# Kernel tuning notes

Measured on AMD Instinct MI355X. Metric: run time of the kernel, lower is better.

The kernel has to match this reference:

```python
import jax, jax.numpy as jnp
import numpy as np

CLAMP_MIN = 1e-6
CLAMP_MAX = 1e6


def setup_inputs() -> dict:
    key = jax.random.key(0)
    k1, k2, k3, k4, k5 = jax.random.split(key, 5)
    R, F, K = 4096, 256, 8
    return {
        "x1": jax.random.normal(k1, (R, F), dtype=jnp.float32),
        "x2": jax.random.normal(k2, (R, F), dtype=jnp.float32),
        "sigmas": jax.random.normal(k3, (K,), dtype=jnp.float32) * 100.0,
        "means": jax.random.normal(k4, (K,), dtype=jnp.float32),
        "sigma_parameters": jax.random.normal(k5, (K,), dtype=jnp.float32),
    }


def reference(x1, x2, sigmas, means, sigma_parameters):
    # dist_k[i,j] = sum_f (x1[i,f] - x2[j,f] - mean_k)^2
    #            = ||x1_i - x2_j||^2 - 2*mean_k*sum_f(x1_i - x2_j) + F*mean_k^2
    # Expansion avoids materializing the R x R x F broadcast tensor.
    R, F = x1.shape
    base = (
        jnp.sum(x1 * x1, axis=1)[:, None]
        + jnp.sum(x2 * x2, axis=1)[None, :]
        - 2.0 * (x1 @ x2.T)
    )  # [R, R]
    s = jnp.sum(x1, axis=1)[:, None] - jnp.sum(x2, axis=1)[None, :]  # [R, R]

    mean = means[:, None, None]  # [K,1,1]
    dist = base[None] - 2.0 * mean * s[None] + jnp.float32(F) * mean * mean  # [K,R,R]
    dist = jnp.clip(dist, CLAMP_MIN, CLAMP_MAX)

    kernel_value = jnp.exp(-dist / (2.0 * sigmas[:, None, None] ** 2))  # [K,R,R]
    softmaxed = jax.nn.softmax(kernel_value, axis=2)  # torch softmax(dim=1) per [R,R]

    weights = 1.0 / (sigma_parameters ** 2)
    normalized_weights = jax.nn.softmax(weights)  # softmax over K
    return jnp.sum(softmaxed * normalized_weights[:, None, None], axis=0)  # [R, R]
```

## Files before the change

### kernel.cpp

```cpp
#include <hip/hip_runtime.h>
#include <cmath>

#define R 4096
#define F 256
#define NK 8

typedef _Float16 half8 __attribute__((ext_vector_type(8)));
typedef _Float16 half4v __attribute__((ext_vector_type(4)));
typedef float f32x4 __attribute__((ext_vector_type(4)));

#define LOG2E      1.4426950408889634f
#define LOG2LOG2E  0.5287663729448977f


__global__ __launch_bounds__(256) void prep_kernel(
    const float* __restrict__ x1, const float* __restrict__ x2,
    const float* __restrict__ sigmas, const float* __restrict__ sigp,
    _Float16* __restrict__ x1h, _Float16* __restrict__ x2h,
    float* __restrict__ r1, float* __restrict__ sq1,
    float* __restrict__ r2, float* __restrict__ sq2,
    float* __restrict__ S, float* __restrict__ prm)
{
    const int tid  = threadIdx.x;
    const int wid  = tid >> 6;
    const int lane = tid & 63;
    const int row  = blockIdx.x * 4 + wid;

    const float* src; _Float16* dsth; float* rs; float* rq; int r;
    if (row < R) { src = x1; dsth = x1h; rs = r1; rq = sq1; r = row; }
    else         { src = x2; dsth = x2h; rs = r2; rq = sq2; r = row - R; }

    float4 v = ((const float4*)(src + (size_t)r * F))[lane];
    half4v h = { (_Float16)v.x, (_Float16)v.y, (_Float16)v.z, (_Float16)v.w };
    *(half4v*)(dsth + (size_t)r * F + lane * 4) = h;

    float s = v.x + v.y + v.z + v.w;
    float q = v.x * v.x + v.y * v.y + v.z * v.z + v.w * v.w;
    for (int m = 1; m < 64; m <<= 1) {
        s += __shfl_xor(s, m);
        q += __shfl_xor(q, m);
    }
    if (lane == 0) { rs[r] = s; rq[r] = q; }

    int g = blockIdx.x * 256 + tid;
    if (g < NK * R) S[g] = 0.f;

    if (blockIdx.x == 0 && tid == 0) {
        float w[NK], mx = -1e30f;
        for (int k = 0; k < NK; ++k) { float sp = sigp[k]; w[k] = 1.f / (sp * sp); mx = fmaxf(mx, w[k]); }
        float sum = 0.f;
        for (int k = 0; k < NK; ++k) { w[k] = expf(w[k] - mx); sum += w[k]; }
        for (int k = 0; k < NK; ++k) prm[k] = w[k] / sum;
        for (int k = 0; k < NK; ++k) {
            float sg = sigmas[k];
            prm[8 + k] = LOG2E / (sg * sg);
        }
    }
}

__global__ __launch_bounds__(256) void prep2_kernel(
    const float* __restrict__ sigmas, const float* __restrict__ means,
    const float* __restrict__ r1, const float* __restrict__ sq1,
    const float* __restrict__ r2, const float* __restrict__ sq2,
    float* __restrict__ rA, float* __restrict__ cB)
{
    int idx  = blockIdx.x * 256 + threadIdx.x;
    int half = idx >> 15;
    int k    = (idx >> 12) & 7;
    int i    = idx & 4095;
    float sg = sigmas[k], m = means[k];
    float c  = -LOG2E / (2.f * sg * sg);
    if (half == 0)
        rA[k * R + i] = c * (sq1[i] - 2.f * m * r1[i] + (float)F * m * m) + LOG2LOG2E;
    else
        cB[k * R + i] = c * (sq2[i] + 2.f * m * r2[i]);
}

__global__ __launch_bounds__(256) void finalize_kernel(
    float* __restrict__ S, const float* __restrict__ prm)
{
    int g = blockIdx.x * 256 + threadIdx.x;
    int k = g >> 12;
    S[g] = prm[k] / S[g];
}

template <int PHASE>
__global__ __launch_bounds__(256, 2) void gemm_kernel(
    const _Float16* __restrict__ Ah, const _Float16* __restrict__ Bh,
    const float* __restrict__ rA, const float* __restrict__ cB,
    const float* __restrict__ prm, float* __restrict__ S, float* __restrict__ out)
{
    constexpr int SK = 72;
    __shared__ _Float16 As[128 * SK];
    __shared__ _Float16 Bs[128 * SK];

    const int tid  = threadIdx.x;
    const int lane = tid & 63;
    const int wid  = tid >> 6;
    const int wm   = wid >> 1, wn = wid & 1;
    const int q    = lane >> 4, m16 = lane & 15;
    const int tm   = blockIdx.y, tn = blockIdx.x;

    f32x4 acc[4][4];
#pragma unroll
    for (int a = 0; a < 4; ++a)
#pragma unroll
        for (int b = 0; b < 4; ++b)
            acc[a][b] = (f32x4){0.f, 0.f, 0.f, 0.f};

    for (int k0 = 0; k0 < F; k0 += 64) {
#pragma unroll
        for (int c = 0; c < 4; ++c) {
            int idx = c * 256 + tid;
            int row = idx >> 3, c8 = (idx & 7) * 8;
            *(uint4*)&As[row * SK + c8] =
                *(const uint4*)&Ah[(size_t)(tm * 128 + row) * F + k0 + c8];
            *(uint4*)&Bs[row * SK + c8] =
                *(const uint4*)&Bh[(size_t)(tn * 128 + row) * F + k0 + c8];
        }
        __syncthreads();
#pragma unroll
        for (int s = 0; s < 2; ++s) {
            half8 a[4], b[4];
#pragma unroll
            for (int mt = 0; mt < 4; ++mt)
                a[mt] = *(const half8*)&As[(wm * 64 + mt * 16 + m16) * SK + s * 32 + q * 8];
#pragma unroll
            for (int nt = 0; nt < 4; ++nt)
                b[nt] = *(const half8*)&Bs[(wn * 64 + nt * 16 + m16) * SK + s * 32 + q * 8];
#pragma unroll
            for (int mt = 0; mt < 4; ++mt)
#pragma unroll
                for (int nt = 0; nt < 4; ++nt)
                    acc[mt][nt] = __builtin_amdgcn_mfma_f32_16x16x32_f16(
                        a[mt], b[nt], acc[mt][nt], 0, 0, 0);
        }
        __syncthreads();
    }

    float g[8];
#pragma unroll
    for (int k = 0; k < 8; ++k) g[k] = prm[8 + k];

    int colg[4];
    float colQ[8][4];
#pragma unroll
    for (int nt = 0; nt < 4; ++nt) {
        colg[nt] = tn * 128 + wn * 64 + nt * 16 + m16;
#pragma unroll
        for (int k = 0; k < 8; ++k) colQ[k][nt] = cB[k * R + colg[nt]];
    }

#pragma unroll
    for (int mt = 0; mt < 4; ++mt) {
#pragma unroll
        for (int r = 0; r < 4; ++r) {
            int rowg = tm * 128 + wm * 64 + mt * 16 + q * 4 + r;
            float rAv[8];
#pragma unroll
            for (int k = 0; k < 8; ++k) rAv[k] = rA[k * R + rowg];

            if (PHASE == 0) {
#pragma unroll
                for (int k = 0; k < 8; ++k) {
                    float t = 0.f;
#pragma unroll
                    for (int nt = 0; nt < 4; ++nt) {
                        float tt = fmaf(g[k], acc[mt][nt][r], rAv[k] + colQ[k][nt]);
                        t += __builtin_amdgcn_exp2f(__builtin_amdgcn_exp2f(tt));
                    }
                    t += __shfl_xor(t, 1); t += __shfl_xor(t, 2);
                    t += __shfl_xor(t, 4); t += __shfl_xor(t, 8);
                    if (m16 == 0) atomicAdd(&S[k * R + rowg], t);
                }
            } else {
                float sv[8];
#pragma unroll
                for (int k = 0; k < 8; ++k) sv[k] = S[k * R + rowg];
#pragma unroll
                for (int nt = 0; nt < 4; ++nt) {
                    float d = acc[mt][nt][r];
                    float o = 0.f;
#pragma unroll
                    for (int k = 0; k < 8; ++k) {
                        float tt = fmaf(g[k], d, rAv[k] + colQ[k][nt]);
                        o = fmaf(sv[k], __builtin_amdgcn_exp2f(__builtin_amdgcn_exp2f(tt)), o);
                    }
                    __builtin_nontemporal_store(o, &out[(size_t)rowg * R + colg[nt]]);
                }
            }
        }
    }
}

extern "C" void kernel_launch(void* const* d_in, const int* in_sizes, int n_in,
                              void* d_out, int out_size, void* d_ws, size_t ws_size,
                              hipStream_t stream) {
    (void)in_sizes; (void)n_in; (void)out_size; (void)ws_size;
    const float* x1     = (const float*)d_in[0];
    const float* x2     = (const float*)d_in[1];
    const float* sigmas = (const float*)d_in[2];
    const float* means  = (const float*)d_in[3];
    const float* sigp   = (const float*)d_in[4];
    float* out = (float*)d_out;

    char* ws = (char*)d_ws;
    _Float16* x1h = (_Float16*)ws;
    _Float16* x2h = (_Float16*)(ws + 2097152);
    float* r1  = (float*)(ws + 4194304);
    float* sq1 = (float*)(ws + 4194304 + 16384);
    float* r2  = (float*)(ws + 4194304 + 32768);
    float* sq2 = (float*)(ws + 4194304 + 49152);
    float* S   = (float*)(ws + 4194304 + 65536);
    float* rA  = (float*)(ws + 4194304 + 196608);
    float* cB  = (float*)(ws + 4194304 + 327680);
    float* prm = (float*)(ws + 4194304 + 458752);

    prep_kernel<<<2048, 256, 0, stream>>>(x1, x2, sigmas, sigp,
                                          x1h, x2h, r1, sq1, r2, sq2, S, prm);
    prep2_kernel<<<256, 256, 0, stream>>>(sigmas, means, r1, sq1, r2, sq2, rA, cB);
    gemm_kernel<0><<<dim3(32, 32), 256, 0, stream>>>(x1h, x2h, rA, cB, prm, S, out);
    finalize_kernel<<<128, 256, 0, stream>>>(S, prm);
    gemm_kernel<1><<<dim3(32, 32), 256, 0, stream>>>(x1h, x2h, rA, cB, prm, S, out);
}
```

Before: 181.9 us.

## Fuse prep2 and finalize into neighbors and prefetch per-row epilogue data

Computes the per-k row and column constants directly in prep_kernel and drops prep2_kernel. The finalize kernel is folded into phase 1 of the GEMM, which computes weight*rcp(S) itself. The epilogue is rewritten as one 16-iteration loop that prefetches the next row's rA/S values, and the phase-0 loop is reordered so each d value is reused across k. This removes two kernel launches and their extra global round-trips. In exchange it adds register pressure and recomputes the reciprocal redundantly in every thread.

```diff
diff --git a/kernel.cpp b/kernel.cpp
--- a/kernel.cpp
+++ b/kernel.cpp
@@ -15,10 +15,10 @@
 
 __global__ __launch_bounds__(256) void prep_kernel(
     const float* __restrict__ x1, const float* __restrict__ x2,
-    const float* __restrict__ sigmas, const float* __restrict__ sigp,
+    const float* __restrict__ sigmas, const float* __restrict__ means,
+    const float* __restrict__ sigp,
     _Float16* __restrict__ x1h, _Float16* __restrict__ x2h,
-    float* __restrict__ r1, float* __restrict__ sq1,
-    float* __restrict__ r2, float* __restrict__ sq2,
+    float* __restrict__ rA, float* __restrict__ cB,
     float* __restrict__ S, float* __restrict__ prm)
 {
     const int tid  = threadIdx.x;
@@ -26,9 +26,9 @@
     const int lane = tid & 63;
     const int row  = blockIdx.x * 4 + wid;
 
-    const float* src; _Float16* dsth; float* rs; float* rq; int r;
-    if (row < R) { src = x1; dsth = x1h; rs = r1; rq = sq1; r = row; }
-    else         { src = x2; dsth = x2h; rs = r2; rq = sq2; r = row - R; }
+    const float* src; _Float16* dsth; int r; bool isX1;
+    if (row < R) { src = x1; dsth = x1h; r = row;     isX1 = true;  }
+    else         { src = x2; dsth = x2h; r = row - R; isX1 = false; }
 
     float4 v = ((const float4*)(src + (size_t)r * F))[lane];
     half4v h = { (_Float16)v.x, (_Float16)v.y, (_Float16)v.z, (_Float16)v.w };
@@ -40,7 +40,13 @@
         s += __shfl_xor(s, m);
         q += __shfl_xor(q, m);
     }
-    if (lane == 0) { rs[r] = s; rq[r] = q; }
+    if (lane < NK) {
+        int k = lane;
+        float sg = sigmas[k], m = means[k];
+        float c  = -LOG2E / (2.f * sg * sg);
+        if (isX1) rA[k * R + r] = c * (q - 2.f * m * s + (float)F * m * m) + LOG2LOG2E;
+        else      cB[k * R + r] = c * (q + 2.f * m * s);
+    }
 
     int g = blockIdx.x * 256 + tid;
     if (g < NK * R) S[g] = 0.f;
@@ -58,32 +64,6 @@
     }
 }
 
-__global__ __launch_bounds__(256) void prep2_kernel(
-    const float* __restrict__ sigmas, const float* __restrict__ means,
-    const float* __restrict__ r1, const float* __restrict__ sq1,
-    const float* __restrict__ r2, const float* __restrict__ sq2,
-    float* __restrict__ rA, float* __restrict__ cB)
-{
-    int idx  = blockIdx.x * 256 + threadIdx.x;
-    int half = idx >> 15;
-    int k    = (idx >> 12) & 7;
-    int i    = idx & 4095;
-    float sg = sigmas[k], m = means[k];
-    float c  = -LOG2E / (2.f * sg * sg);
-    if (half == 0)
-        rA[k * R + i] = c * (sq1[i] - 2.f * m * r1[i] + (float)F * m * m) + LOG2LOG2E;
-    else
-        cB[k * R + i] = c * (sq2[i] + 2.f * m * r2[i]);
-}
-
-__global__ __launch_bounds__(256) void finalize_kernel(
-    float* __restrict__ S, const float* __restrict__ prm)
-{
-    int g = blockIdx.x * 256 + threadIdx.x;
-    int k = g >> 12;
-    S[g] = prm[k] / S[g];
-}
-
 template <int PHASE>
 __global__ __launch_bounds__(256, 2) void gemm_kernel(
     const _Float16* __restrict__ Ah, const _Float16* __restrict__ Bh,
@@ -138,9 +118,13 @@
         __syncthreads();
     }
 
-    float g[8];
+    float g[8], wv[8];
 #pragma unroll
     for (int k = 0; k < 8; ++k) g[k] = prm[8 + k];
+    if (PHASE == 1) {
+#pragma unroll
+        for (int k = 0; k < 8; ++k) wv[k] = prm[k];
+    }
 
     int colg[4];
     float colQ[8][4];
@@ -151,43 +135,73 @@
         for (int k = 0; k < 8; ++k) colQ[k][nt] = cB[k * R + colg[nt]];
     }
 
-#pragma unroll
-    for (int mt = 0; mt < 4; ++mt) {
-#pragma unroll
-        for (int r = 0; r < 4; ++r) {
-            int rowg = tm * 128 + wm * 64 + mt * 16 + q * 4 + r;
-            float rAv[8];
-#pragma unroll
-            for (int k = 0; k < 8; ++k) rAv[k] = rA[k * R + rowg];
-
-            if (PHASE == 0) {
+    const int rowb = tm * 128 + wm * 64 + q * 4;
+    float rAv[8], Sv[8];
+#pragma unroll
+    for (int k = 0; k < 8; ++k) {
+        rAv[k] = rA[k * R + rowb];
+        if (PHASE == 1) Sv[k] = S[k * R + rowb];
+    }
+
+#pragma unroll
+    for (int it = 0; it < 16; ++it) {
+        const int mt = it >> 2, r = it & 3;
+        const int rowg = rowb + mt * 16 + r;
+
+        float rAn[8], Sn[8];
+        if (it < 15) {
+            const int itn = it + 1;
+            const int rowgn = rowb + (itn >> 2) * 16 + (itn & 3);
+#pragma unroll
+            for (int k = 0; k < 8; ++k) {
+                rAn[k] = rA[k * R + rowgn];
+                if (PHASE == 1) Sn[k] = S[k * R + rowgn];
+            }
+        }
+
+        if (PHASE == 0) {
+            float tk[8];
+#pragma unroll
+            for (int k = 0; k < 8; ++k) tk[k] = 0.f;
+#pragma unroll
+            for (int nt = 0; nt < 4; ++nt) {
+                float d = acc[mt][nt][r];
 #pragma unroll
                 for (int k = 0; k < 8; ++k) {
-                    float t = 0.f;
-#pragma unroll
-                    for (int nt = 0; nt < 4; ++nt) {
-                        float tt = fmaf(g[k], acc[mt][nt][r], rAv[k] + colQ[k][nt]);
-                        t += __builtin_amdgcn_exp2f(__builtin_amdgcn_exp2f(tt));
-                    }
-                    t += __shfl_xor(t, 1); t += __shfl_xor(t, 2);
-                    t += __shfl_xor(t, 4); t += __shfl_xor(t, 8);
-                    if (m16 == 0) atomicAdd(&S[k * R + rowg], t);
+                    float t = fmaf(g[k], d, rAv[k] + colQ[k][nt]);
+                    tk[k] += __builtin_amdgcn_exp2f(__builtin_amdgcn_exp2f(t));
                 }
-            } else {
-                float sv[8];
-#pragma unroll
-                for (int k = 0; k < 8; ++k) sv[k] = S[k * R + rowg];
-#pragma unroll
-                for (int nt = 0; nt < 4; ++nt) {
-                    float d = acc[mt][nt][r];
-                    float o = 0.f;
-#pragma unroll
-                    for (int k = 0; k < 8; ++k) {
-                        float tt = fmaf(g[k], d, rAv[k] + colQ[k][nt]);
-                        o = fmaf(sv[k], __builtin_amdgcn_exp2f(__builtin_amdgcn_exp2f(tt)), o);
-                    }
-                    __builtin_nontemporal_store(o, &out[(size_t)rowg * R + colg[nt]]);
+            }
+#pragma unroll
+            for (int k = 0; k < 8; ++k) {
+                float t = tk[k];
+                t += __shfl_xor(t, 1); t += __shfl_xor(t, 2);
+                t += __shfl_xor(t, 4); t += __shfl_xor(t, 8);
+                if (m16 == 0) atomicAdd(&S[k * R + rowg], t);
+            }
+        } else {
+            float sv[8];
+#pragma unroll
+            for (int k = 0; k < 8; ++k)
+                sv[k] = wv[k] * __builtin_amdgcn_rcpf(Sv[k]);
+#pragma unroll
+            for (int nt = 0; nt < 4; ++nt) {
+                float d = acc[mt][nt][r];
+                float o = 0.f;
+#pragma unroll
+                for (int k = 0; k < 8; ++k) {
+                    float t = fmaf(g[k], d, rAv[k] + colQ[k][nt]);
+                    o = fmaf(sv[k], __builtin_amdgcn_exp2f(__builtin_amdgcn_exp2f(t)), o);
                 }
+                __builtin_nontemporal_store(o, &out[(size_t)rowg * R + colg[nt]]);
+            }
+        }
+
+        if (it < 15) {
+#pragma unroll
+            for (int k = 0; k < 8; ++k) {
+                rAv[k] = rAn[k];
+                if (PHASE == 1) Sv[k] = Sn[k];
             }
         }
     }
@@ -207,19 +221,13 @@
     char* ws = (char*)d_ws;
     _Float16* x1h = (_Float16*)ws;
     _Float16* x2h = (_Float16*)(ws + 2097152);
-    float* r1  = (float*)(ws + 4194304);
-    float* sq1 = (float*)(ws + 4194304 + 16384);
-    float* r2  = (float*)(ws + 4194304 + 32768);
-    float* sq2 = (float*)(ws + 4194304 + 49152);
-    float* S   = (float*)(ws + 4194304 + 65536);
-    float* rA  = (float*)(ws + 4194304 + 196608);
-    float* cB  = (float*)(ws + 4194304 + 327680);
-    float* prm = (float*)(ws + 4194304 + 458752);
-
-    prep_kernel<<<2048, 256, 0, stream>>>(x1, x2, sigmas, sigp,
-                                          x1h, x2h, r1, sq1, r2, sq2, S, prm);
-    prep2_kernel<<<256, 256, 0, stream>>>(sigmas, means, r1, sq1, r2, sq2, rA, cB);
+    float* S   = (float*)(ws + 4194304);
+    float* rA  = (float*)(ws + 4194304 + 131072);
+    float* cB  = (float*)(ws + 4194304 + 262144);
+    float* prm = (float*)(ws + 4194304 + 393216);
+
+    prep_kernel<<<2048, 256, 0, stream>>>(x1, x2, sigmas, means, sigp,
+                                          x1h, x2h, rA, cB, S, prm);
     gemm_kernel<0><<<dim3(32, 32), 256, 0, stream>>>(x1h, x2h, rA, cB, prm, S, out);
-    finalize_kernel<<<128, 256, 0, stream>>>(S, prm);
     gemm_kernel<1><<<dim3(32, 32), 256, 0, stream>>>(x1h, x2h, rA, cB, prm, S, out);
 }
```

New measurement: 186.1 us. +2.3%, slower.
